# Kernel tuning notes

Measured on AMD Instinct MI355X. Metric: run time of the kernel, lower is better.

## Reference

```python
import jax, jax.numpy as jnp
import numpy as np

EMBED_DIM = 200
INPUT_DIM = 512


def setup_inputs() -> dict:
    key = jax.random.key(0)
    k1, k2, k3, k4 = jax.random.split(key, 4)
    B, L, T = 64, 256, 64
    x = jax.random.normal(k1, (B, L, INPUT_DIM), dtype=jnp.float32)
    y = jax.random.normal(k2, (B, T, INPUT_DIM), dtype=jnp.float32)
    # fc = nn.Linear(input_dim, embedding_dim)
    W = jax.random.normal(k3, (EMBED_DIM, INPUT_DIM), dtype=jnp.float32) * (1.0 / np.sqrt(INPUT_DIM))
    b = jax.random.normal(k4, (EMBED_DIM,), dtype=jnp.float32) * 0.01
    return {"x": x, "y": y, "W": W, "b": b}


def reference(x, y, W, b):
    # Project both modalities (last dim != embedding_dim in original triggers fc)
    xp = jnp.einsum('bld,ed->ble', x, W) + b   # B x L x E
    yp = jnp.einsum('btd,ed->bte', y, W) + b   # B x T x E
    # Pairwise matchmap: for pair (i, j), matchmap = xp[i] @ yp[j].T -> L x T
    mm = jnp.einsum('ile,jte->ijlt', xp, yp)   # B x B x L x T
    # MISA: max over L (rows of matchmap, dim 0), then mean over T
    S = jnp.max(mm, axis=2).mean(axis=2)       # B x B
    return S
```

## Files before the change

kernel.cpp:

```cpp
#include <hip/hip_runtime.h>
#include <hip/hip_bf16.h>
#include <stdint.h>

#define BB 64
#define LL 256
#define TT 64
#define DD 512
#define EE 200
#define EP 208
#define NKK 13
#define NROWS_X 16384
#define YCH_PER_J (2 * NKK * 64)
#define BSTRIDE 264

typedef __attribute__((ext_vector_type(8))) short short8;
typedef __attribute__((ext_vector_type(4))) float floatx4;
typedef __attribute__((ext_vector_type(16))) float floatx16;
typedef __attribute__((ext_vector_type(4))) int intx4;

__device__ __forceinline__ short f2bf(float f) {
  uint32_t u = __builtin_bit_cast(uint32_t, f);
  u = (u + 0x7fffu + ((u >> 16) & 1u)) >> 16;
  return (short)u;
}

__device__ __forceinline__ uint32_t pack2(float lo, float hi) {
  return __builtin_amdgcn_perm(__builtin_bit_cast(uint32_t, hi),
                               __builtin_bit_cast(uint32_t, lo), 0x07060302u);
}

typedef const __attribute__((address_space(1))) uint32_t gu32_t;
typedef __attribute__((address_space(3))) uint32_t lu32_t;
__device__ __forceinline__ void glds16(const void* g, void* l) {
  __builtin_amdgcn_global_load_lds((gu32_t*)g, (lu32_t*)l, 16, 0, 0);
}

__global__ void wcvt_kernel(const float* __restrict__ W, short* __restrict__ Wb) {
  int idx = blockIdx.x * 256 + threadIdx.x;
  int e = idx >> 9;
  int k = idx & 511;
  float v = (e < EE) ? W[e * DD + k] : 0.0f;
  Wb[idx] = f2bf(v);
}

__global__ __launch_bounds__(256, 3) void proj_kernel(const float* __restrict__ x,
                                                      const float* __restrict__ y,
                                                      const short* __restrict__ Wb,
                                                      const float* __restrict__ bias,
                                                      short* __restrict__ pT) {
  __shared__ __align__(16) char smem[43008];
  float* ldsA = (float*)smem;
  short* ldsB = (short*)(smem + 16384);
  short* bounce = (short*)smem;

  const int tid  = threadIdx.x;
  const int lane = tid & 63;
  const int wid  = tid >> 6;
  const int r16   = lane & 15;
  const int khalf = lane >> 4;

  const int row0 = blockIdx.x * 64;
  const float* srcbase = (row0 < NROWS_X) ? (x + (size_t)row0 * DD)
                                          : (y + (size_t)(row0 - NROWS_X) * DD);

  floatx4 acc[NKK];
#pragma unroll
  for (int n = 0; n < NKK; n++) acc[n] = (floatx4){0.f, 0.f, 0.f, 0.f};

  auto stage = [&](int buf, int ks) {
#pragma unroll
    for (int it = 0; it < 2; it++) {
      const int p = it * 256 + tid;
      const int r = p >> 3, c = p & 7;
      glds16(srcbase + (size_t)r * DD + ks * 32 + ((c ^ (r & 7)) << 2),
             &ldsA[buf * 2048 + p * 4]);
    }
#pragma unroll
    for (int it = 0; it < 4; it++) {
      const int p = it * 256 + tid;
      if (p < 832) {
        const int r = p >> 2, c = p & 3;
        glds16(Wb + (size_t)r * DD + ks * 32 + ((c ^ (r & 3)) << 3),
               &ldsB[buf * 6656 + p * 8]);
      }
    }
  };

  stage(0, 0);

  for (int s = 0; s < 16; s++) {
    __syncthreads();
    if (s + 1 < 16) stage((s + 1) & 1, s + 1);

    const int buf = s & 1;
    const int r = wid * 16 + r16;
    const int c0 = (2 * khalf) ^ (r & 7);
    const int c1 = (2 * khalf + 1) ^ (r & 7);
    const floatx4 f0 = *(const floatx4*)&ldsA[buf * 2048 + r * 32 + c0 * 4];
    const floatx4 f1 = *(const floatx4*)&ldsA[buf * 2048 + r * 32 + c1 * 4];
    union { short8 s8; uint32_t u[4]; } af;
    af.u[0] = pack2(f0.x, f0.y);
    af.u[1] = pack2(f0.z, f0.w);
    af.u[2] = pack2(f1.x, f1.y);
    af.u[3] = pack2(f1.z, f1.w);
#pragma unroll
    for (int n = 0; n < NKK; n++) {
      const int erow = n * 16 + r16;
      const short8 bfrag = *(const short8*)&ldsB[buf * 6656 + erow * 32 + ((khalf ^ (erow & 3)) << 3)];
      acc[n] = __builtin_amdgcn_mfma_f32_16x16x32_bf16(af.s8, bfrag, acc[n], 0, 0, 0);
    }
  }

  __syncthreads();

#pragma unroll
  for (int n = 0; n < NKK; n++) {
    const int e = n * 16 + r16;
    const float bv = (e < EE) ? bias[e] : 0.0f;
#pragma unroll
    for (int rr = 0; rr < 4; rr++) {
      const int lr = wid * 16 + khalf * 4 + rr;
      bounce[lr * BSTRIDE + e] = f2bf(acc[n][rr] + bv);
    }
  }
  __syncthreads();

  const int rowblk0 = row0 >> 5;
  for (int c = tid; c < 1664; c += 256) {
    const int q  = c >> 6;
    const int mt = (q >= 13) ? 1 : 0;
    const int n  = q - mt * 13;
    const int l  = c & 63;
    const int lr = mt * 32 + (l & 31);
    const short8 piece = *(const short8*)&bounce[lr * BSTRIDE + n * 16 + (l >> 5) * 8];
    *(short8*)&pT[((size_t)((rowblk0 + mt) * 13 + n)) * 512 + l * 8] = piece;
  }
}

__global__ __launch_bounds__(512, 2) void pair_kernel(const short* __restrict__ xpT,
                                                      const short* __restrict__ ypT,
                                                      float* __restrict__ S) {
  __shared__ __align__(16) char ldsbuf[106496 + 16384];
  short* ylds = (short*)ldsbuf;
  float* red  = (float*)(ldsbuf + 106496);

  const int tid  = threadIdx.x;
  const int lane = tid & 63;
  const int wid  = tid >> 6;
  const int wq   = wid & 3;
  const int jh   = wid >> 2;
  const int ibase = (blockIdx.x >> 4) * 4;
  const int j0    = (blockIdx.x & 15) * 4;

  {
    const short* src = ypT + (size_t)j0 * YCH_PER_J * 8;
    for (int c = tid; c < 4 * YCH_PER_J; c += 512) {
      glds16(src + (size_t)c * 8, ldsbuf + c * 16);
    }
  }
  __syncthreads();

  for (int ii = 0; ii < 4; ii++) {
    const int i = ibase + ii;

    floatx16 acc[2][2][2];
#pragma unroll
    for (int jjj = 0; jjj < 2; jjj++)
#pragma unroll
      for (int m = 0; m < 2; m++)
#pragma unroll
        for (int nt = 0; nt < 2; nt++)
#pragma unroll
          for (int r = 0; r < 16; r++) acc[jjj][m][nt][r] = 0.f;

    const short* a0base = xpT + ((size_t)((i * 8 + wq * 2 + 0) * NKK) * 512) + lane * 8;
    const short* a1base = xpT + ((size_t)((i * 8 + wq * 2 + 1) * NKK) * 512) + lane * 8;

#pragma unroll
    for (int kk = 0; kk < NKK; kk++) {
      const short8 a0 = *(const short8*)(a0base + kk * 512);
      const short8 a1 = *(const short8*)(a1base + kk * 512);
#pragma unroll
      for (int jjj = 0; jjj < 2; jjj++) {
#pragma unroll
        for (int nt = 0; nt < 2; nt++) {
          const int jl = jh * 2 + jjj;
          const short8 bf = *(const short8*)(ylds + ((size_t)((jl * 2 + nt) * NKK + kk)) * 512 + lane * 8);
          acc[jjj][0][nt] = __builtin_amdgcn_mfma_f32_32x32x16_bf16(a0, bf, acc[jjj][0][nt], 0, 0, 0);
          acc[jjj][1][nt] = __builtin_amdgcn_mfma_f32_32x32x16_bf16(a1, bf, acc[jjj][1][nt], 0, 0, 0);
        }
      }
    }

#pragma unroll
    for (int jjj = 0; jjj < 2; jjj++) {
#pragma unroll
      for (int nt = 0; nt < 2; nt++) {
        float v = acc[jjj][0][nt][0];
#pragma unroll
        for (int m = 0; m < 2; m++)
#pragma unroll
          for (int r = 0; r < 16; r++) v = fmaxf(v, acc[jjj][m][nt][r]);
        v = fmaxf(v, __shfl_xor(v, 32, 64));
        if (lane < 32) {
          const int jl = jh * 2 + jjj;
          red[((wq * 4 + ii) * 4 + jl) * 64 + nt * 32 + lane] = v;
        }
      }
    }
  }
  __syncthreads();

#pragma unroll
  for (int w2 = 0; w2 < 2; w2++) {
    const int combo = wid * 2 + w2;
    const int ii = combo >> 2;
    const int jl = combo & 3;
    const int t  = lane;
    float v = red[((0 * 4 + ii) * 4 + jl) * 64 + t];
    v = fmaxf(v, red[((1 * 4 + ii) * 4 + jl) * 64 + t]);
    v = fmaxf(v, red[((2 * 4 + ii) * 4 + jl) * 64 + t]);
    v = fmaxf(v, red[((3 * 4 + ii) * 4 + jl) * 64 + t]);
    v += __shfl_xor(v, 1, 64);
    v += __shfl_xor(v, 2, 64);
    v += __shfl_xor(v, 4, 64);
    v += __shfl_xor(v, 8, 64);
    v += __shfl_xor(v, 16, 64);
    v += __shfl_xor(v, 32, 64);
    if (t == 0) S[(ibase + ii) * BB + j0 + jl] = v * (1.0f / 64.0f);
  }
}

extern "C" void kernel_launch(void* const* d_in, const int* in_sizes, int n_in,
                              void* d_out, int out_size, void* d_ws, size_t ws_size,
                              hipStream_t stream) {
  const float* x = (const float*)d_in[0];
  const float* y = (const float*)d_in[1];
  const float* W = (const float*)d_in[2];
  const float* b = (const float*)d_in[3];
  float* S = (float*)d_out;

  char* ws = (char*)d_ws;
  short* Wb = (short*)ws;
  short* pT = (short*)(ws + 262144);
  short* ypT = pT + (size_t)6656 * 512;

  wcvt_kernel<<<416, 256, 0, stream>>>(W, Wb);
  proj_kernel<<<320, 256, 0, stream>>>(x, y, Wb, b, pT);
  pair_kernel<<<256, 512, 0, stream>>>(pT, ypT, S);
}
```

Before: 48.94 us.

## Triple-buffer projection loads, widen pair kernel to 1024 threads, vectorize W conversion

The projection kernel moves from double to triple buffering, using vmcnt-based barriers so two stages of loads can be in flight while computing. The W-row staging is made unconditional by clamping rows, and LDS grows to 72KB, which caps occupancy at 2 blocks. The pair kernel now uses 16 waves, each handling one j instead of two, with a swizzled block-to-(i,j) mapping for cache locality. The W bf16 conversion is vectorized to 8 elements per thread.

Result: slower. 53.26 us (+8.8%).

```diff
diff --git a/kernel.cpp b/kernel.cpp
--- a/kernel.cpp
+++ b/kernel.cpp
@@ -16,7 +16,6 @@
 typedef __attribute__((ext_vector_type(8))) short short8;
 typedef __attribute__((ext_vector_type(4))) float floatx4;
 typedef __attribute__((ext_vector_type(16))) float floatx16;
-typedef __attribute__((ext_vector_type(4))) int intx4;
 
 __device__ __forceinline__ short f2bf(float f) {
   uint32_t u = __builtin_bit_cast(uint32_t, f);
@@ -35,22 +34,32 @@
   __builtin_amdgcn_global_load_lds((gu32_t*)g, (lu32_t*)l, 16, 0, 0);
 }
 
+#define VMCNT_BARRIER(N) asm volatile("s_waitcnt vmcnt(" #N ")\n\ts_barrier" ::: "memory")
+
 __global__ void wcvt_kernel(const float* __restrict__ W, short* __restrict__ Wb) {
-  int idx = blockIdx.x * 256 + threadIdx.x;
-  int e = idx >> 9;
-  int k = idx & 511;
-  float v = (e < EE) ? W[e * DD + k] : 0.0f;
-  Wb[idx] = f2bf(v);
-}
-
-__global__ __launch_bounds__(256, 3) void proj_kernel(const float* __restrict__ x,
+  const int t = blockIdx.x * 256 + threadIdx.x;
+  const int base = t * 8;
+  const int e = base >> 9;
+  union { short8 s8; uint32_t u[4]; } o;
+  if (e < EE) {
+    const floatx4 f0 = *(const floatx4*)(W + base);
+    const floatx4 f1 = *(const floatx4*)(W + base + 4);
+    o.u[0] = pack2(f0.x, f0.y); o.u[1] = pack2(f0.z, f0.w);
+    o.u[2] = pack2(f1.x, f1.y); o.u[3] = pack2(f1.z, f1.w);
+  } else {
+    o.u[0] = o.u[1] = o.u[2] = o.u[3] = 0u;
+  }
+  *(short8*)(Wb + base) = o.s8;
+}
+
+__global__ __launch_bounds__(256, 2) void proj_kernel(const float* __restrict__ x,
                                                       const float* __restrict__ y,
                                                       const short* __restrict__ Wb,
                                                       const float* __restrict__ bias,
                                                       short* __restrict__ pT) {
-  __shared__ __align__(16) char smem[43008];
+  __shared__ __align__(16) char smem[73728];
   float* ldsA = (float*)smem;
-  short* ldsB = (short*)(smem + 16384);
+  short* ldsB = (short*)(smem + 24576);
   short* bounce = (short*)smem;
 
   const int tid  = threadIdx.x;
@@ -78,21 +87,15 @@
 #pragma unroll
     for (int it = 0; it < 4; it++) {
       const int p = it * 256 + tid;
-      if (p < 832) {
-        const int r = p >> 2, c = p & 3;
-        glds16(Wb + (size_t)r * DD + ks * 32 + ((c ^ (r & 3)) << 3),
-               &ldsB[buf * 6656 + p * 8]);
-      }
+      const int r = p >> 2, c = p & 3;
+      const int sr = (r < EP) ? r : (EP - 1);
+      glds16(Wb + (size_t)sr * DD + ks * 32 + ((c ^ (r & 3)) << 3),
+             &ldsB[buf * 8192 + p * 8]);
     }
   };
 
-  stage(0, 0);
-
-  for (int s = 0; s < 16; s++) {
-    __syncthreads();
-    if (s + 1 < 16) stage((s + 1) & 1, s + 1);
-
-    const int buf = s & 1;
+  auto compute = [&](int s) {
+    const int buf = s % 3;
     const int r = wid * 16 + r16;
     const int c0 = (2 * khalf) ^ (r & 7);
     const int c1 = (2 * khalf + 1) ^ (r & 7);
@@ -106,10 +109,21 @@
 #pragma unroll
     for (int n = 0; n < NKK; n++) {
       const int erow = n * 16 + r16;
-      const short8 bfrag = *(const short8*)&ldsB[buf * 6656 + erow * 32 + ((khalf ^ (erow & 3)) << 3)];
+      const short8 bfrag = *(const short8*)&ldsB[buf * 8192 + erow * 32 + ((khalf ^ (erow & 3)) << 3)];
       acc[n] = __builtin_amdgcn_mfma_f32_16x16x32_bf16(af.s8, bfrag, acc[n], 0, 0, 0);
     }
-  }
+  };
+
+  stage(0, 0);
+  stage(1, 1);
+
+  for (int s = 0; s < 15; s++) {
+    VMCNT_BARRIER(6);
+    if (s + 2 < 16) stage((s + 2) % 3, s + 2);
+    compute(s);
+  }
+  VMCNT_BARRIER(0);
+  compute(15);
 
   __syncthreads();
 
@@ -137,9 +151,9 @@
   }
 }
 
-__global__ __launch_bounds__(512, 2) void pair_kernel(const short* __restrict__ xpT,
-                                                      const short* __restrict__ ypT,
-                                                      float* __restrict__ S) {
+__global__ __launch_bounds__(1024, 4) void pair_kernel(const short* __restrict__ xpT,
+                                                       const short* __restrict__ ypT,
+                                                       float* __restrict__ S) {
   __shared__ __align__(16) char ldsbuf[106496 + 16384];
   short* ylds = (short*)ldsbuf;
   float* red  = (float*)(ldsbuf + 106496);
@@ -148,13 +162,16 @@
   const int lane = tid & 63;
   const int wid  = tid >> 6;
   const int wq   = wid & 3;
-  const int jh   = wid >> 2;
-  const int ibase = (blockIdx.x >> 4) * 4;
-  const int j0    = (blockIdx.x & 15) * 4;
+  const int jw   = wid >> 2;
+  const int bid  = blockIdx.x;
+  const int igrp = ((bid & 7) << 1) | ((bid >> 3) & 1);
+  const int jgrp = bid >> 4;
+  const int ibase = igrp * 4;
+  const int j0    = jgrp * 4;
 
   {
     const short* src = ypT + (size_t)j0 * YCH_PER_J * 8;
-    for (int c = tid; c < 4 * YCH_PER_J; c += 512) {
+    for (int c = tid; c < 4 * YCH_PER_J; c += 1024) {
       glds16(src + (size_t)c * 8, ldsbuf + c * 16);
     }
   }
@@ -163,15 +180,13 @@
   for (int ii = 0; ii < 4; ii++) {
     const int i = ibase + ii;
 
-    floatx16 acc[2][2][2];
-#pragma unroll
-    for (int jjj = 0; jjj < 2; jjj++)
-#pragma unroll
-      for (int m = 0; m < 2; m++)
-#pragma unroll
-        for (int nt = 0; nt < 2; nt++)
-#pragma unroll
-          for (int r = 0; r < 16; r++) acc[jjj][m][nt][r] = 0.f;
+    floatx16 acc[2][2];
+#pragma unroll
+    for (int m = 0; m < 2; m++)
+#pragma unroll
+      for (int nt = 0; nt < 2; nt++)
+#pragma unroll
+        for (int r = 0; r < 16; r++) acc[m][nt][r] = 0.f;
 
     const short* a0base = xpT + ((size_t)((i * 8 + wq * 2 + 0) * NKK) * 512) + lane * 8;
     const short* a1base = xpT + ((size_t)((i * 8 + wq * 2 + 1) * NKK) * 512) + lane * 8;
@@ -181,41 +196,30 @@
       const short8 a0 = *(const short8*)(a0base + kk * 512);
       const short8 a1 = *(const short8*)(a1base + kk * 512);
 #pragma unroll
-      for (int jjj = 0; jjj < 2; jjj++) {
-#pragma unroll
-        for (int nt = 0; nt < 2; nt++) {
-          const int jl = jh * 2 + jjj;
-          const short8 bf = *(const short8*)(ylds + ((size_t)((jl * 2 + nt) * NKK + kk)) * 512 + lane * 8);
-          acc[jjj][0][nt] = __builtin_amdgcn_mfma_f32_32x32x16_bf16(a0, bf, acc[jjj][0][nt], 0, 0, 0);
-          acc[jjj][1][nt] = __builtin_amdgcn_mfma_f32_32x32x16_bf16(a1, bf, acc[jjj][1][nt], 0, 0, 0);
-        }
+      for (int nt = 0; nt < 2; nt++) {
+        const short8 bf = *(const short8*)(ylds + ((size_t)((jw * 2 + nt) * NKK + kk)) * 512 + lane * 8);
+        acc[0][nt] = __builtin_amdgcn_mfma_f32_32x32x16_bf16(a0, bf, acc[0][nt], 0, 0, 0);
+        acc[1][nt] = __builtin_amdgcn_mfma_f32_32x32x16_bf16(a1, bf, acc[1][nt], 0, 0, 0);
       }
     }
 
 #pragma unroll
-    for (int jjj = 0; jjj < 2; jjj++) {
-#pragma unroll
-      for (int nt = 0; nt < 2; nt++) {
-        float v = acc[jjj][0][nt][0];
-#pragma unroll
-        for (int m = 0; m < 2; m++)
-#pragma unroll
-          for (int r = 0; r < 16; r++) v = fmaxf(v, acc[jjj][m][nt][r]);
-        v = fmaxf(v, __shfl_xor(v, 32, 64));
-        if (lane < 32) {
-          const int jl = jh * 2 + jjj;
-          red[((wq * 4 + ii) * 4 + jl) * 64 + nt * 32 + lane] = v;
-        }
-      }
-    }
-  }
-  __syncthreads();
-
-#pragma unroll
-  for (int w2 = 0; w2 < 2; w2++) {
-    const int combo = wid * 2 + w2;
-    const int ii = combo >> 2;
-    const int jl = combo & 3;
+    for (int nt = 0; nt < 2; nt++) {
+      float v = acc[0][nt][0];
+#pragma unroll
+      for (int m = 0; m < 2; m++)
+#pragma unroll
+        for (int r = 0; r < 16; r++) v = fmaxf(v, acc[m][nt][r]);
+      v = fmaxf(v, __shfl_xor(v, 32, 64));
+      if (lane < 32)
+        red[((wq * 4 + ii) * 4 + jw) * 64 + nt * 32 + lane] = v;
+    }
+  }
+  __syncthreads();
+
+  {
+    const int ii = wid >> 2;
+    const int jl = wid & 3;
     const int t  = lane;
     float v = red[((0 * 4 + ii) * 4 + jl) * 64 + t];
     v = fmaxf(v, red[((1 * 4 + ii) * 4 + jl) * 64 + t]);
@@ -245,7 +249,7 @@
   short* pT = (short*)(ws + 262144);
   short* ypT = pT + (size_t)6656 * 512;
 
-  wcvt_kernel<<<416, 256, 0, stream>>>(W, Wb);
+  wcvt_kernel<<<52, 256, 0, stream>>>(W, Wb);
   proj_kernel<<<320, 256, 0, stream>>>(x, y, Wb, b, pT);
-  pair_kernel<<<256, 512, 0, stream>>>(pT, ypT, S);
-}
+  pair_kernel<<<256, 1024, 0, stream>>>(pT, ypT, S);
+}
```
